# Kernel tuning notes

Hardware: AMD Instinct MI355X
Metric: run time of the kernel (lower is better)

## Reference

```python
import jax, jax.numpy as jnp
import numpy as np

N_NODES = 100000
N_EDGES = 1000000
N_RELS = 8
N_HEADS = 4
IN_FEAT = 64
OUT_FEAT = 64
D_HEAD = OUT_FEAT // N_HEADS
LEAKY_SLOPE = 0.2


def setup_inputs() -> dict:
    key = jax.random.key(0)
    ks = jax.random.split(key, 8)
    x = jax.random.normal(ks[0], (N_NODES, IN_FEAT), dtype=jnp.float32)
    src_idx = jax.random.randint(ks[1], (N_EDGES,), 0, N_NODES)
    dst_idx = jax.random.randint(ks[2], (N_EDGES,), 0, N_NODES)
    edge_rel = jnp.sort(jax.random.randint(ks[3], (N_EDGES,), 0, N_RELS))
    # xavier-ish small init for weights
    conv_weights = jax.random.normal(ks[4], (N_RELS, N_HEADS, IN_FEAT, D_HEAD), dtype=jnp.float32) * 0.1
    attn_l = jax.random.normal(ks[5], (N_RELS, N_HEADS, D_HEAD), dtype=jnp.float32) * 0.1
    attn_r = jax.random.normal(ks[6], (N_RELS, N_HEADS, D_HEAD), dtype=jnp.float32) * 0.1
    h_bias = jnp.zeros((OUT_FEAT,), dtype=jnp.float32)
    return {
        'x': x, 'src_idx': src_idx, 'dst_idx': dst_idx, 'edge_rel': edge_rel,
        'conv_weights': conv_weights, 'attn_l': attn_l, 'attn_r': attn_r,
        'h_bias': h_bias,
    }


def reference(x, src_idx, dst_idx, edge_rel, conv_weights, attn_l, attn_r, h_bias):
    N = x.shape[0]
    # Per-relation transform of all node features: [R, N, H, D]
    feat_all = jnp.einsum('ni,rhid->rnhd', x, conv_weights)
    # Per-relation attention logits per node: [R, N, H]
    el_all = jnp.einsum('rnhd,rhd->rnh', feat_all, attn_l)
    er_all = jnp.einsum('rnhd,rhd->rnh', feat_all, attn_r)
    # Gather per-edge quantities (relation-specific transform of src/dst)
    feat_e = feat_all[edge_rel, src_idx]          # [E, H, D]
    el = el_all[edge_rel, src_idx]                # [E, H]
    er = er_all[edge_rel, dst_idx]                # [E, H]
    s = jax.nn.leaky_relu(el + er, negative_slope=LEAKY_SLOPE)
    # Edge softmax over incoming edges of each destination node (per head)
    m = jax.ops.segment_max(s, dst_idx, num_segments=N)      # [N, H]
    e = jnp.exp(s - m[dst_idx])                               # [E, H]
    denom = jax.ops.segment_sum(e, dst_idx, num_segments=N)   # [N, H]
    w = e / jnp.maximum(denom[dst_idx], jnp.float32(1e-16))   # [E, H]
    # Weighted aggregation of source features into destination nodes
    agg = jax.ops.segment_sum(feat_e * w[..., None], dst_idx, num_segments=N)  # [N, H, D]
    h = agg.reshape(N, OUT_FEAT) + h_bias
    # activation=None, dropout in eval mode -> identity
    return h
```

## Files before the change

kernel.cpp:

```cpp
#include <hip/hip_runtime.h>
#include <hip/hip_bf16.h>

#define NN 100000
#define NE 1000000
#define NR 8

#define EB 1024
#define NBLK 977
#define NBUCK 196
#define NT (NBUCK*NBLK)
#define NBB 749

#define K3DPB 32
#define K3CAP 160

#define K0_BLKS  160
#define PRE_BLKS (K0_BLKS + NBLK)

typedef unsigned short u16;
typedef unsigned int u32;
typedef __attribute__((ext_vector_type(8))) short bf16x8;
typedef __attribute__((ext_vector_type(4))) float f32x4;

static __device__ __forceinline__ float bf2f(u16 u) {
    union { u32 i; float f; } v; v.i = ((u32)u) << 16; return v.f;
}
static __device__ __forceinline__ float bflo(u32 u) {
    union { u32 i; float f; } v; v.i = u << 16; return v.f;
}
static __device__ __forceinline__ float bfhi(u32 u) {
    union { u32 i; float f; } v; v.i = u & 0xffff0000u; return v.f;
}
static __device__ __forceinline__ u16 f2bf(float f) {
    __hip_bfloat16 h = __float2bfloat16(f);
    return *reinterpret_cast<u16*>(&h);
}
static __device__ __forceinline__ float ldf(const void* p, int idx, int isf32) {
    return isf32 ? ((const float*)p)[idx] : bf2f(((const u16*)p)[idx]);
}

static __device__ __forceinline__ int detect_wave(const u16* xw, int lane)
{
    int insane = 0;
    for (int k = lane; k < 512; k += 64) {
        u16 w = xw[k];
        int ex = (w >> 7) & 0xFF;
        bool sane = ((w & 0x7FFF) == 0) || (ex >= 96 && ex <= 159);
        insane += sane ? 0 : 1;
    }
    for (int off = 32; off; off >>= 1) insane += __shfl_down(insane, off);
    return insane;
}

__global__ __launch_bounds__(256) void k_pre(
    const void* __restrict__ xin, int* __restrict__ flag,
    const void* __restrict__ cw, const void* __restrict__ al,
    const void* __restrict__ ar, u16* __restrict__ Bpre,
    const int* __restrict__ dsti, int* __restrict__ histT)
{
    __shared__ int sflag;
    __shared__ int hist[NBUCK];
    int t = threadIdx.x;
    int b = blockIdx.x;

    if (b < K0_BLKS) {
        if (t < 64) {
            int insane = detect_wave((const u16*)xin, t);
            if (t == 0) {
                sflag = (insane > 50) ? 1 : 0;
                if (b == 0) *flag = sflag;
            }
        }
        __syncthreads();
        int isf32 = sflag;
        int tid = b * 256 + t;
        if (tid >= NR * 5120) return;
        int r = tid / 5120, rem = tid % 5120;
        int c = rem >> 3, j = rem & 7;
        int nt = c >> 7, kk = (c >> 6) & 1, lc = c & 63;
        int i = kk * 32 + ((lc >> 4) << 3) + j;
        int d = lc & 15;
        u16 val;
        if (nt < 4) {
            val = f2bf(ldf(cw, ((r * 4 + nt) * 64 + i) * 16 + d, isf32));
        } else if (d < 8) {
            int h = d >> 1;
            const void* attn = (d & 1) ? ar : al;
            float s = 0.f;
            for (int dd = 0; dd < 16; ++dd)
                s += ldf(cw, ((r * 4 + h) * 64 + i) * 16 + dd, isf32)
                   * ldf(attn, (r * 4 + h) * 16 + dd, isf32);
            val = f2bf(s);
        } else {
            val = 0;
        }
        Bpre[tid] = val;
    } else {
        int blk = b - K0_BLKS;
        if (t < NBUCK) hist[t] = 0;
        __syncthreads();
        int base = blk * EB;
        for (int j = 0; j < EB; j += 256) {
            int e = base + j + t;
            if (e < NE) atomicAdd(&hist[dsti[e] >> 9], 1);
        }
        __syncthreads();
        if (t < NBUCK) histT[t * NBLK + blk] = hist[t];
    }
}

__global__ __launch_bounds__(256) void k1_feat(
    const void* __restrict__ xin, const u16* __restrict__ Bpre,
    u16* __restrict__ feat_all, float* __restrict__ el_all, float* __restrict__ er_all)
{
    __shared__ int sflag;
    __shared__ alignas(16) u16 ldsA[4096];
    __shared__ alignas(16) u16 ldsF[2][4096];
    int n0 = blockIdx.x * 64;
    int tid = threadIdx.x;
    int wave = tid >> 6, lane = tid & 63;
    int col = lane & 15, quad = lane >> 4;

    if (tid < 64) {
        int insane = detect_wave((const u16*)xin, tid);
        if (tid == 0) sflag = (insane > 50) ? 1 : 0;
    }
    __syncthreads();
    int isf32 = sflag;

    for (int c = tid; c < 512; c += 256) {
        int mt = c >> 7, kk = (c >> 6) & 1, lc = c & 63;
        int node = n0 + mt * 16 + (lc & 15);
        if (node >= NN) node = NN - 1;
        int kbase = kk * 32 + ((lc >> 4) << 3);
        if (!isf32) {
            *(uint4*)&ldsA[c * 8] = *(const uint4*)&((const u16*)xin)[node * 64 + kbase];
        } else {
            const f32x4* xf4 = (const f32x4*)((const float*)xin + node * 64 + kbase);
            f32x4 a = xf4[0], b = xf4[1];
            uint4 o;
            o.x = (u32)f2bf(a[0]) | ((u32)f2bf(a[1]) << 16);
            o.y = (u32)f2bf(a[2]) | ((u32)f2bf(a[3]) << 16);
            o.z = (u32)f2bf(b[0]) | ((u32)f2bf(b[1]) << 16);
            o.w = (u32)f2bf(b[2]) | ((u32)f2bf(b[3]) << 16);
            *(uint4*)&ldsA[c * 8] = o;
        }
    }
    __syncthreads();
    bf16x8 afrag0 = *(bf16x8*)&ldsA[((wave * 2 + 0) * 64 + lane) * 8];
    bf16x8 afrag1 = *(bf16x8*)&ldsA[((wave * 2 + 1) * 64 + lane) * 8];

    for (int r = 0; r < NR; ++r) {
        int buf = r & 1;
        f32x4 acc[5];
#pragma unroll
        for (int nt = 0; nt < 5; ++nt) acc[nt] = f32x4{0.f, 0.f, 0.f, 0.f};
#pragma unroll
        for (int nt = 0; nt < 5; ++nt) {
            bf16x8 b0 = *(const bf16x8*)&Bpre[r * 5120 + ((nt * 2 + 0) * 64 + lane) * 8];
            bf16x8 b1 = *(const bf16x8*)&Bpre[r * 5120 + ((nt * 2 + 1) * 64 + lane) * 8];
            acc[nt] = __builtin_amdgcn_mfma_f32_16x16x32_bf16(afrag0, b0, acc[nt], 0, 0, 0);
            acc[nt] = __builtin_amdgcn_mfma_f32_16x16x32_bf16(afrag1, b1, acc[nt], 0, 0, 0);
        }

        if (col < 8) {
            int h = col >> 1;
            float* dstp = (col & 1) ? er_all : el_all;
#pragma unroll
            for (int reg = 0; reg < 4; ++reg) {
                int node = n0 + wave * 16 + quad * 4 + reg;
                if (node < NN) dstp[(r * NN + node) * 4 + h] = acc[4][reg];
            }
        }
#pragma unroll
        for (int nt = 0; nt < 4; ++nt) {
            int cg = nt * 16 + col;
#pragma unroll
            for (int reg = 0; reg < 4; ++reg) {
                int row = quad * 4 + reg;
                ldsF[buf][(wave * 16 + row) * 64 + cg] = f2bf(acc[nt][reg]);
            }
        }
        __syncthreads();
        for (int c = tid; c < 512; c += 256) {
            int nl = c >> 3, part = c & 7;
            int node = n0 + nl;
            if (node < NN)
                *(uint4*)&feat_all[(r * NN + node) * 64 + part * 8] = *(uint4*)&ldsF[buf][c * 8];
        }
    }
}

__global__ __launch_bounds__(256) void k_scanB1(int* __restrict__ histT,
                                                int* __restrict__ bsum)
{
    __shared__ int wtot[4];
    int t = threadIdx.x;
    int gi = blockIdx.x * 256 + t;
    int v = (gi < NT) ? histT[gi] : 0;
    int lane = t & 63, w = t >> 6;
    int s = v;
#pragma unroll
    for (int m = 1; m < 64; m <<= 1) {
        int u = __shfl_up(s, m);
        if (lane >= m) s += u;
    }
    if (lane == 63) wtot[w] = s;
    __syncthreads();
    int wb = 0;
    for (int i = 0; i < w; ++i) wb += wtot[i];
    if (gi < NT) histT[gi] = wb + s - v;
    if (t == 255) bsum[blockIdx.x] = wb + s;
}

__global__ __launch_bounds__(1024) void k_scanB2(const int* __restrict__ bsum,
                                                 int* __restrict__ boff,
                                                 const int* __restrict__ histT,
                                                 int* __restrict__ bstart)
{
    __shared__ int wtot[16];
    __shared__ int sboff[NBB];
    int t = threadIdx.x;
    int v = (t < NBB) ? bsum[t] : 0;
    int lane = t & 63, w = t >> 6;
    int s = v;
#pragma unroll
    for (int m = 1; m < 64; m <<= 1) {
        int u = __shfl_up(s, m);
        if (lane >= m) s += u;
    }
    if (lane == 63) wtot[w] = s;
    __syncthreads();
    int wb = 0;
    for (int i = 0; i < w; ++i) wb += wtot[i];
    if (t < NBB) {
        int val = wb + s - v;
        boff[t] = val;
        sboff[t] = val;
    }
    __syncthreads();
    if (t < NBUCK) {
        int gi = t * NBLK;
        bstart[t] = histT[gi] + sboff[gi >> 8];
    }
    if (t == 0) bstart[NBUCK] = NE;
}

__global__ __launch_bounds__(256) void k_binC(
    const int* __restrict__ srci, const int* __restrict__ dsti,
    const int* __restrict__ reli, const int* __restrict__ histT,
    const int* __restrict__ boff, int* __restrict__ key_b)
{
    __shared__ int cur[NBUCK];
    int t = threadIdx.x, blk = blockIdx.x;
    if (t < NBUCK) {
        int gi = t * NBLK + blk;
        cur[t] = histT[gi] + boff[gi >> 8];
    }
    __syncthreads();
    int base = blk * EB;
    for (int j = 0; j < EB; j += 256) {
        int e = base + j + t;
        if (e < NE) {
            int d = dsti[e];
            int key = ((d & 511) << 20) | (reli[e] << 17) | srci[e];
            int pos = atomicAdd(&cur[d >> 9], 1);
            key_b[pos] = key;
        }
    }
}

__global__ __launch_bounds__(1024) void k_binD(
    const int* __restrict__ bstart, const int* __restrict__ key_b,
    int* __restrict__ key_s, int* __restrict__ off)
{
    __shared__ int cnt[512];
    __shared__ int wtot[8];
    int t = threadIdx.x, b = blockIdx.x;
    int s0 = bstart[b], s1 = bstart[b + 1];
    if (t < 512) cnt[t] = 0;
    __syncthreads();
    for (int j = s0 + t; j < s1; j += 1024)
        atomicAdd(&cnt[(key_b[j] >> 20) & 511], 1);
    __syncthreads();
    int excl = 0;
    if (t < 512) {
        int v = cnt[t];
        int lane = t & 63, w = t >> 6;
        int s = v;
#pragma unroll
        for (int m = 1; m < 64; m <<= 1) {
            int u = __shfl_up(s, m);
            if (lane >= m) s += u;
        }
        if (lane == 63) wtot[w] = s;
        __syncthreads();
        int wb = 0;
        for (int i = 0; i < w; ++i) wb += wtot[i];
        excl = s0 + wb + s - v;
        int d = (b << 9) + t;
        if (d < NN) off[d] = excl;
    } else {
        __syncthreads();
    }
    __syncthreads();
    if (t < 512) cnt[t] = excl;
    if (b == 0 && t == 0) off[NN] = NE;
    __syncthreads();
    for (int j = s0 + t; j < s1; j += 1024) {
        int key = key_b[j];
        int pos = atomicAdd(&cnt[(key >> 20) & 511], 1);
        key_s[pos] = key;
    }
}

__global__ __launch_bounds__(256) void k3_node(
    const int* __restrict__ off, const int* __restrict__ key_s,
    const float* __restrict__ el_all, const float* __restrict__ er_all,
    const u16* __restrict__ feat_all, const void* __restrict__ bias,
    const int* __restrict__ flag, void* __restrict__ out)
{
    __shared__ int   ldsOffs[K3DPB + 1];
    __shared__ int   ldsKey[4][K3CAP];
    __shared__ float ldsEE[4][K3CAP][4];
    int t = threadIdx.x;
    int wave = t >> 6, lane = t & 63;
    int dg = lane >> 3;
    int fl = lane & 7;
    int h  = fl >> 1;
    int d0 = blockIdx.x * K3DPB;
    int isf32 = *flag;

    if (t < K3DPB + 1) ldsOffs[t] = off[min(d0 + t, NN)];
    __syncthreads();

    int dlo = wave * 8;
    int estart = ldsOffs[dlo], eend = ldsOffs[dlo + 8];
    int scount = min(eend - estart, K3CAP);

    int dbase = d0 & ~511;
    for (int j = lane; j < scount; j += 64) {
        int key = key_s[estart + j];
        int rel = (key >> 17) & 7, src = key & 131071;
        int d = dbase | ((key >> 20) & 511);
        int kk = rel * NN + src;
        f32x4 el = *(const f32x4*)&el_all[kk * 4];
        f32x4 er = *(const f32x4*)&er_all[(rel * NN + d) * 4];
        f32x4 ee;
#pragma unroll
        for (int q = 0; q < 4; ++q) {
            float v = el[q] + er[q];
            v = v > 0.f ? v : 0.2f * v;
            ee[q] = __expf(v);
        }
        ldsKey[wave][j] = kk;
        *(f32x4*)&ldsEE[wave][j][0] = ee;
    }

    float bv[8];
#pragma unroll
    for (int q = 0; q < 8; ++q) bv[q] = ldf(bias, fl * 8 + q, isf32);

    int nl = dlo + dg;
    int d = d0 + nl;
    int s  = ldsOffs[nl] - estart;
    int e1 = ldsOffs[nl + 1] - estart;
    float acc[8] = {0.f, 0.f, 0.f, 0.f, 0.f, 0.f, 0.f, 0.f};
    float accW = 0.f;

    int e1c = min(e1, K3CAP);
    for (int base = s; base < e1c; base += 4) {
        int kk[4]; float w[4];
#pragma unroll
        for (int q = 0; q < 4; ++q) {
            int idx = base + q;
            bool vld = idx < e1c;
            kk[q] = vld ? ldsKey[wave][idx] : 0;
            w[q]  = vld ? ldsEE[wave][idx][h] : 0.f;
        }
        uint4 u[4];
#pragma unroll
        for (int q = 0; q < 4; ++q)
            u[q] = *(const uint4*)&feat_all[kk[q] * 64 + fl * 8];
#pragma unroll
        for (int q = 0; q < 4; ++q) {
            acc[0] += bflo(u[q].x) * w[q];
            acc[1] += bfhi(u[q].x) * w[q];
            acc[2] += bflo(u[q].y) * w[q];
            acc[3] += bfhi(u[q].y) * w[q];
            acc[4] += bflo(u[q].z) * w[q];
            acc[5] += bfhi(u[q].z) * w[q];
            acc[6] += bflo(u[q].w) * w[q];
            acc[7] += bfhi(u[q].w) * w[q];
            accW += w[q];
        }
    }
    for (int j = max(s, K3CAP); j < e1; ++j) {
        int key = key_s[estart + j];
        int rel = (key >> 17) & 7, src = key & 131071;
        int kk0 = rel * NN + src;
        float v = el_all[kk0 * 4 + h] + er_all[(rel * NN + d) * 4 + h];
        v = v > 0.f ? v : 0.2f * v;
        float w0 = __expf(v);
        uint4 u = *(const uint4*)&feat_all[kk0 * 64 + fl * 8];
        acc[0] += bflo(u.x) * w0;
        acc[1] += bfhi(u.x) * w0;
        acc[2] += bflo(u.y) * w0;
        acc[3] += bfhi(u.y) * w0;
        acc[4] += bflo(u.z) * w0;
        acc[5] += bfhi(u.z) * w0;
        acc[6] += bflo(u.w) * w0;
        acc[7] += bfhi(u.w) * w0;
        accW += w0;
    }

    {
        float invh = 1.f / fmaxf(accW, 1e-16f);
        float o[8];
#pragma unroll
        for (int q = 0; q < 8; ++q) o[q] = acc[q] * invh + bv[q];
        if (isf32) {
            ((f32x4*)out)[d * 16 + fl * 2]     = f32x4{o[0], o[1], o[2], o[3]};
            ((f32x4*)out)[d * 16 + fl * 2 + 1] = f32x4{o[4], o[5], o[6], o[7]};
        } else {
            uint4 st;
            st.x = (u32)f2bf(o[0]) | ((u32)f2bf(o[1]) << 16);
            st.y = (u32)f2bf(o[2]) | ((u32)f2bf(o[3]) << 16);
            st.z = (u32)f2bf(o[4]) | ((u32)f2bf(o[5]) << 16);
            st.w = (u32)f2bf(o[6]) | ((u32)f2bf(o[7]) << 16);
            *(uint4*)&((u16*)out)[d * 64 + fl * 8] = st;
        }
    }
}

extern "C" void kernel_launch(void* const* d_in, const int* in_sizes, int n_in,
                              void* d_out, int out_size, void* d_ws, size_t ws_size,
                              hipStream_t stream)
{
    const void* x   = d_in[0];
    const int* srci = (const int*)d_in[1];
    const int* dsti = (const int*)d_in[2];
    const int* reli = (const int*)d_in[3];
    const void* cw  = d_in[4];
    const void* al  = d_in[5];
    const void* ar  = d_in[6];
    const void* hb  = d_in[7];

    char* ws = (char*)d_ws;
    u16*   feat_all = (u16*)  (ws + 0);
    float* el_all   = (float*)(ws + 102400000);
    float* er_all   = (float*)(ws + 115200000);
    int*   key_s    = (int*)  (ws + 128000000);
    int*   key_b    = (int*)  (ws + 132000000);
    int*   off      = (int*)  (ws + 136000000);
    int*   histT    = (int*)  (ws + 136400064);
    int*   bsum     = (int*)  (ws + 137166032);
    int*   boff     = (int*)  (ws + 137169040);
    int*   bstart   = (int*)  (ws + 137172048);
    u16*   Bpre     = (u16*)  (ws + 137172880);
    int*   flag     = (int*)  (ws + 137254800);

    k_pre<<<PRE_BLKS, 256, 0, stream>>>(x, flag, cw, al, ar, Bpre, dsti, histT);
    k1_feat<<<(NN + 63) / 64, 256, 0, stream>>>(x, Bpre, feat_all, el_all, er_all);
    k_scanB1<<<NBB, 256, 0, stream>>>(histT, bsum);
    k_scanB2<<<1, 1024, 0, stream>>>(bsum, boff, histT, bstart);
    k_binC<<<NBLK, 256, 0, stream>>>(srci, dsti, reli, histT, boff, key_b);
    k_binD<<<NBUCK, 1024, 0, stream>>>(bstart, key_b, key_s, off);
    k3_node<<<(NN + 31) / 32, 256, 0, stream>>>(off, key_s, el_all, er_all, feat_all,
                                                hb, flag, d_out);
}
```

Measured before the change: 203.0 us.

## Split feature kernel across relation groups and store MFMA results directly

The feature-transform kernel now launches four times as many blocks, each handling two relations for a 64-node chunk instead of all eight. The MFMA operands are swapped so each lane holds a node's output columns, which lets results be written straight to global memory as packed bf16 and float2 stores. This drops the LDS staging buffer and per-relation barrier. The cost is that the input tile is reloaded and converted four times, and the direct stores are narrower and less coalesced than the previous 16-byte staged writes.

```diff
diff --git a/kernel.cpp b/kernel.cpp
--- a/kernel.cpp
+++ b/kernel.cpp
@@ -13,6 +13,9 @@
 
 #define K3DPB 32
 #define K3CAP 160
+
+#define K1RPB 2
+#define K1GROUPS (NR / K1RPB)
 
 #define K0_BLKS  160
 #define PRE_BLKS (K0_BLKS + NBLK)
@@ -115,8 +118,9 @@
 {
     __shared__ int sflag;
     __shared__ alignas(16) u16 ldsA[4096];
-    __shared__ alignas(16) u16 ldsF[2][4096];
-    int n0 = blockIdx.x * 64;
+    int chunk = blockIdx.x >> 2;
+    int r0 = (blockIdx.x & 3) * K1RPB;
+    int n0 = chunk * 64;
     int tid = threadIdx.x;
     int wave = tid >> 6, lane = tid & 63;
     int col = lane & 15, quad = lane >> 4;
@@ -129,8 +133,8 @@
     int isf32 = sflag;
 
     for (int c = tid; c < 512; c += 256) {
-        int mt = c >> 7, kk = (c >> 6) & 1, lc = c & 63;
-        int node = n0 + mt * 16 + (lc & 15);
+        int kk = (c >> 6) & 1, lc = c & 63;
+        int node = n0 + (c >> 7) * 16 + (lc & 15);
         if (node >= NN) node = NN - 1;
         int kbase = kk * 32 + ((lc >> 4) << 3);
         if (!isf32) {
@@ -150,8 +154,12 @@
     bf16x8 afrag0 = *(bf16x8*)&ldsA[((wave * 2 + 0) * 64 + lane) * 8];
     bf16x8 afrag1 = *(bf16x8*)&ldsA[((wave * 2 + 1) * 64 + lane) * 8];
 
-    for (int r = 0; r < NR; ++r) {
-        int buf = r & 1;
+    int node = n0 + wave * 16 + col;
+    bool nvalid = node < NN;
+
+#pragma unroll
+    for (int rr = 0; rr < K1RPB; ++rr) {
+        int r = r0 + rr;
         f32x4 acc[5];
 #pragma unroll
         for (int nt = 0; nt < 5; ++nt) acc[nt] = f32x4{0.f, 0.f, 0.f, 0.f};
@@ -159,34 +167,24 @@
         for (int nt = 0; nt < 5; ++nt) {
             bf16x8 b0 = *(const bf16x8*)&Bpre[r * 5120 + ((nt * 2 + 0) * 64 + lane) * 8];
             bf16x8 b1 = *(const bf16x8*)&Bpre[r * 5120 + ((nt * 2 + 1) * 64 + lane) * 8];
-            acc[nt] = __builtin_amdgcn_mfma_f32_16x16x32_bf16(afrag0, b0, acc[nt], 0, 0, 0);
-            acc[nt] = __builtin_amdgcn_mfma_f32_16x16x32_bf16(afrag1, b1, acc[nt], 0, 0, 0);
-        }
-
-        if (col < 8) {
-            int h = col >> 1;
-            float* dstp = (col & 1) ? er_all : el_all;
-#pragma unroll
-            for (int reg = 0; reg < 4; ++reg) {
-                int node = n0 + wave * 16 + quad * 4 + reg;
-                if (node < NN) dstp[(r * NN + node) * 4 + h] = acc[4][reg];
+            acc[nt] = __builtin_amdgcn_mfma_f32_16x16x32_bf16(b0, afrag0, acc[nt], 0, 0, 0);
+            acc[nt] = __builtin_amdgcn_mfma_f32_16x16x32_bf16(b1, afrag1, acc[nt], 0, 0, 0);
+        }
+
+        if (nvalid) {
+            int fb = (r * NN + node) * 64;
+#pragma unroll
+            for (int nt = 0; nt < 4; ++nt) {
+                uint2 st;
+                st.x = (u32)f2bf(acc[nt][0]) | ((u32)f2bf(acc[nt][1]) << 16);
+                st.y = (u32)f2bf(acc[nt][2]) | ((u32)f2bf(acc[nt][3]) << 16);
+                *(uint2*)&feat_all[fb + nt * 16 + quad * 4] = st;
             }
-        }
-#pragma unroll
-        for (int nt = 0; nt < 4; ++nt) {
-            int cg = nt * 16 + col;
-#pragma unroll
-            for (int reg = 0; reg < 4; ++reg) {
-                int row = quad * 4 + reg;
-                ldsF[buf][(wave * 16 + row) * 64 + cg] = f2bf(acc[nt][reg]);
+            if (quad < 2) {
+                int eb = (r * NN + node) * 4 + quad * 2;
+                *(float2*)&el_all[eb] = float2{acc[4][0], acc[4][2]};
+                *(float2*)&er_all[eb] = float2{acc[4][1], acc[4][3]};
             }
-        }
-        __syncthreads();
-        for (int c = tid; c < 512; c += 256) {
-            int nl = c >> 3, part = c & 7;
-            int node = n0 + nl;
-            if (node < NN)
-                *(uint4*)&feat_all[(r * NN + node) * 64 + part * 8] = *(uint4*)&ldsF[buf][c * 8];
         }
     }
 }
@@ -461,7 +459,7 @@
     int*   flag     = (int*)  (ws + 137254800);
 
     k_pre<<<PRE_BLKS, 256, 0, stream>>>(x, flag, cw, al, ar, Bpre, dsti, histT);
-    k1_feat<<<(NN + 63) / 64, 256, 0, stream>>>(x, Bpre, feat_all, el_all, er_all);
+    k1_feat<<<((NN + 63) / 64) * K1GROUPS, 256, 0, stream>>>(x, Bpre, feat_all, el_all, er_all);
     k_scanB1<<<NBB, 256, 0, stream>>>(histT, bsum);
     k_scanB2<<<1, 1024, 0, stream>>>(bsum, boff, histT, bstart);
     k_binC<<<NBLK, 256, 0, stream>>>(srci, dsti, reli, histT, boff, key_b);
```

New measurement: 225.0 us. 1.11x slower.
